# Optimization experiments

Hardware: AMD Instinct MI355X
Metric: run time of the kernel (lower is better)

The kernel has to match this reference:

```python
import jax, jax.numpy as jnp
import numpy as np

HEAD_NUM = 16
QKV_DIM = 32
EMB = 512
SQRT_EMB = 22.627416997969522  # sqrt(512)
LOGIT_CLIP = 10.0
BATCH, POMO, PROBLEM = 32, 256, 1024


def setup_inputs() -> dict:
    key = jax.random.key(0)
    ks = jax.random.split(key, 8)
    s = 0.02
    return {
        "encoded_nodes": jax.random.normal(ks[0], (BATCH, PROBLEM, EMB), jnp.float32),
        "encoded_q1": jax.random.normal(ks[1], (BATCH, POMO, EMB), jnp.float32),
        "encoded_last_node": jax.random.normal(ks[2], (BATCH, POMO, EMB), jnp.float32),
        "ninf_mask": jnp.zeros((BATCH, POMO, PROBLEM), jnp.float32),
        # weights stored [in, out] so y = x @ W (equiv. to torch Linear with W.T)
        "Wq_first": jax.random.normal(ks[3], (EMB, HEAD_NUM * QKV_DIM), jnp.float32) * s,
        "Wq_last": jax.random.normal(ks[4], (EMB, HEAD_NUM * QKV_DIM), jnp.float32) * s,
        "Wk": jax.random.normal(ks[5], (EMB, HEAD_NUM * QKV_DIM), jnp.float32) * s,
        "Wv": jax.random.normal(ks[6], (EMB, HEAD_NUM * QKV_DIM), jnp.float32) * s,
        "W_combine": jax.random.normal(ks[7], (HEAD_NUM * QKV_DIM, EMB), jnp.float32) * s,
        "b_combine": jnp.zeros((EMB,), jnp.float32),
    }


def _heads(x):
    # [b, n, h*d] -> [b, h, n, d]
    b, n, _ = x.shape
    return x.reshape(b, n, HEAD_NUM, QKV_DIM).transpose(0, 2, 1, 3)


def reference(encoded_nodes, encoded_q1, encoded_last_node, ninf_mask,
              Wq_first, Wq_last, Wk, Wv, W_combine, b_combine):
    # set_kv
    k = _heads(encoded_nodes @ Wk)                     # [b,h,problem,d]
    v = _heads(encoded_nodes @ Wv)                     # [b,h,problem,d]
    single_head_key = encoded_nodes.transpose(0, 2, 1) # [b,emb,problem]
    # set_q1
    q_first = _heads(encoded_q1 @ Wq_first)            # [b,h,pomo,d]
    # forward
    q_last = _heads(encoded_last_node @ Wq_last)       # [b,h,pomo,d]
    q = q_first + q_last

    scale = 1.0 / jnp.sqrt(jnp.asarray(QKV_DIM, q.dtype))
    score = jnp.einsum("bhnd,bhmd->bhnm", q, k) * scale  # [b,h,pomo,problem]
    score = score + ninf_mask[:, None, :, :]
    weights = jax.nn.softmax(score, axis=-1)
    out = jnp.einsum("bhnm,bhmd->bhnd", weights, v)      # [b,h,pomo,d]
    out_concat = out.transpose(0, 2, 1, 3).reshape(q.shape[0], q.shape[2], HEAD_NUM * QKV_DIM)
    mh_out = out_concat @ W_combine + b_combine          # [b,pomo,emb]

    score2 = jnp.einsum("bne,bem->bnm", mh_out, single_head_key) / SQRT_EMB
    score2 = LOGIT_CLIP * jnp.tanh(score2) + ninf_mask
    probs = jax.nn.softmax(score2, axis=2)               # [b,pomo,problem]
    return probs
```

## Files before the change

### kernel.cpp

```cpp
#include <hip/hip_runtime.h>
#include <math.h>

typedef unsigned short u16;
typedef __attribute__((ext_vector_type(8))) short bf16x8;
typedef __attribute__((ext_vector_type(4))) float f32x4;
typedef __attribute__((ext_vector_type(4))) int i32x4;
typedef __attribute__((ext_vector_type(4))) short s16x4;
typedef __attribute__((ext_vector_type(4))) unsigned short u16x4;

#define MFMA16(a,b,c) __builtin_amdgcn_mfma_f32_16x16x32_bf16((a),(b),(c),0,0,0)

__device__ __forceinline__ u16 f2bf(float x){
  unsigned int u = __float_as_uint(x);
  u += 0x7fffu + ((u >> 16) & 1u);
  return (u16)(u >> 16);
}
__device__ __forceinline__ float bf2f(u16 x){
  return __uint_as_float(((unsigned)x) << 16);
}
__device__ __forceinline__ void gload16(const void* g, void* l){
  __builtin_amdgcn_global_load_lds((const __attribute__((address_space(1))) void*)g,
                                   (__attribute__((address_space(3))) void*)l, 16, 0, 0);
}

__global__ __launch_bounds__(256) void prep(
    const float* __restrict__ nodes, const float* __restrict__ q1, const float* __restrict__ lastn,
    const float* __restrict__ mask,
    const float* __restrict__ Wqf, const float* __restrict__ Wql, const float* __restrict__ Wk,
    const float* __restrict__ Wv, const float* __restrict__ Wc,
    u16* __restrict__ nodesb, u16* __restrict__ qlb,
    u16* __restrict__ WtKV, u16* __restrict__ WtQ2, u16* __restrict__ WtC,
    u16* __restrict__ maskP)
{
  const int tid = blockIdx.x * 256 + threadIdx.x;
  const int NT = 1048576;
  for (int i = tid; i < 4194304; i += NT) {
    float4 v = ((const float4*)nodes)[i];
    u16x4 o; o[0]=f2bf(v.x); o[1]=f2bf(v.y); o[2]=f2bf(v.z); o[3]=f2bf(v.w);
    *(u16x4*)&nodesb[i*4] = o;
  }
  {
    const int m = tid >> 7, k4 = (tid & 127)*4;
    float4 v = ((const float4*)q1)[tid];
    u16x4 o; o[0]=f2bf(v.x); o[1]=f2bf(v.y); o[2]=f2bf(v.z); o[3]=f2bf(v.w);
    *(u16x4*)&qlb[m*1024 + k4] = o;
    v = ((const float4*)lastn)[tid];
    o[0]=f2bf(v.x); o[1]=f2bf(v.y); o[2]=f2bf(v.z); o[3]=f2bf(v.w);
    *(u16x4*)&qlb[m*1024 + 512 + k4] = o;
  }
  if (tid < 262144) {
    int n = tid >> 9, k = tid & 511;
    WtQ2[n*1024 + k]       = f2bf(Wqf[k*512 + n]);
    WtQ2[n*1024 + 512 + k] = f2bf(Wql[k*512 + n]);
    WtC[tid]  = f2bf(Wc[k*512 + n]);
  }
  if (tid < 524288) {
    int n = tid >> 9, k = tid & 511;
    WtKV[tid] = f2bf(n < 512 ? Wk[k*512 + n] : Wv[k*512 + (n-512)]);
  }
  if (tid < 524288) {
    int brt = tid >> 10, c = tid & 1023;
    const float* mp = mask + (brt*16)*1024 + c;
    u16 vals[16];
    #pragma unroll
    for (int p=0;p<16;p++) vals[p] = f2bf(mp[p*1024]);
    *(i32x4*)&maskP[tid*16]     = *(i32x4*)&vals[0];
    *(i32x4*)&maskP[tid*16 + 8] = *(i32x4*)&vals[8];
  }
}

__global__ __launch_bounds__(512, 2) void kvq(
    const u16* __restrict__ Akv, const u16* __restrict__ Bkv,
    const u16* __restrict__ Aq,  const u16* __restrict__ Bq,
    u16* __restrict__ Kout, u16* __restrict__ Vout, u16* __restrict__ Qout)
{
  __shared__ u16 smem[24576];
  const int t = threadIdx.x, w = t >> 6, l = t & 63, q = l >> 4, ln = l & 15;
  const int wr = w >> 2, wc = w & 3;
  const int wm = wr * 64, wn = wc * 64;

  const bool isq = blockIdx.x < 128;
  int mb, nb, ksteps, kstr;
  const u16 *Ab, *Bb;
  if (isq) {
    const int bid = blockIdx.x;
    mb = bid >> 1; nb = bid & 1;
    ksteps = 32; kstr = 1024; Ab = Aq; Bb = Bq;
  } else {
    const int bid = blockIdx.x - 128;
    mb = (bid >> 5)*8 + (bid & 7);
    nb = (bid >> 3) & 3;
    ksteps = 16; kstr = 512; Ab = Akv; Bb = Bkv;
  }
  const int m0 = mb*128, n0 = nb*256;

  f32x4 acc[4][4];
  #pragma unroll
  for (int i=0;i<4;i++)
    #pragma unroll
    for (int j=0;j<4;j++)
      #pragma unroll
      for (int r=0;r<4;r++) acc[i][j][r] = 0.f;

  const u16* Aaddr = Ab + (m0 + (t & 127))*kstr + (t >> 7)*8;
  const u16* Baddr = Bb + (n0 + (t & 255))*kstr + (t >> 8)*8;

  #define STAGE(kc_, b_) { \
    u16* s = smem + (b_)*12288; \
    gload16(Aaddr + (kc_)*32,      &s[t*8]); \
    gload16(Baddr + (kc_)*32,      &s[4096 + t*8]); \
    gload16(Baddr + 16 + (kc_)*32, &s[4096 + (t+512)*8]); }

  STAGE(0, 0);
  for (int kc = 0; kc < ksteps; kc++) {
    __syncthreads();
    if (kc + 1 < ksteps) STAGE(kc+1, (kc+1)&1);
    const u16* sa = smem + (kc&1)*12288;
    const u16* sb = sa + 4096;
    bf16x8 af[4], bfr[4];
    #pragma unroll
    for (int i=0;i<4;i++) af[i]  = *(bf16x8*)&sa[(q*128 + wm + i*16 + ln)*8];
    #pragma unroll
    for (int j=0;j<4;j++) bfr[j] = *(bf16x8*)&sb[(q*256 + wn + j*16 + ln)*8];
    #pragma unroll
    for (int i=0;i<4;i++)
      #pragma unroll
      for (int j=0;j<4;j++)
        acc[i][j] = MFMA16(af[i], bfr[j], acc[i][j]);
  }
  #undef STAGE

  const float scale = isq ? 0.17677669529663687f : 1.0f;
  const int bb_ = mb >> 3, mloc = (mb & 7)*128;
  const int bbq = mb >> 1, pm0 = (mb & 1)*128;
  for (int h = 0; h < 4; ++h) {
    __syncthreads();
    if (wc == h) {
      #pragma unroll
      for (int i=0;i<4;i++)
        #pragma unroll
        for (int j=0;j<4;j++) {
          s16x4 o;
          #pragma unroll
          for (int r=0;r<4;r++) o[r] = (short)f2bf(acc[i][j][r]*scale);
          *(s16x4*)&smem[(j*16 + ln)*140 + wm + i*16 + q*4] = o;
        }
    }
    __syncthreads();
    #pragma unroll
    for (int hc=0; hc<2; ++hc) {
      if (isq) {
        const int head = nb*8 + h*2 + hc;
        const int m_ = t >> 2, d0 = (t & 3)*8;
        u16 v[8];
        #pragma unroll
        for (int dd=0;dd<8;dd++) v[dd] = smem[(hc*32 + d0 + dd)*140 + m_];
        *(i32x4*)&Qout[((bbq*16 + head)*256 + pm0 + m_)*32 + d0] = *(i32x4*)&v[0];
      } else if (nb < 2) {
        const int head = nb*8 + h*2 + hc;
        const int m_ = t >> 2, d0 = (t & 3)*8;
        u16 v[8];
        #pragma unroll
        for (int dd=0;dd<8;dd++) v[dd] = smem[(hc*32 + d0 + dd)*140 + m_];
        *(i32x4*)&Kout[((bb_*16 + head)*1024 + mloc + m_)*32 + d0] = *(i32x4*)&v[0];
      } else {
        const int vh = (nb-2)*8 + h*2 + hc;
        const int d = t >> 4, mo = (t & 15)*8;
        *(i32x4*)&Vout[((bb_*16 + vh)*32 + d)*1024 + mloc + mo]
            = *(i32x4*)&smem[(hc*32 + d)*140 + mo];
      }
    }
  }
}

__global__ __launch_bounds__(256) void attn(const u16* __restrict__ Qg, const u16* __restrict__ Kg,
                                            const u16* __restrict__ Vtg, const u16* __restrict__ maskP,
                                            u16* __restrict__ Og)
{
  const int bid = blockIdx.x;
  const int bh = (bid & 7)*64 + (bid >> 3);
  const int h = bh & 15, bb = bh >> 4;
  const int t = threadIdx.x, w = t >> 6, l = t & 63, q = l >> 4, ln = l & 15;
  __shared__ u16 Qs[8192];
  __shared__ u16 Ks[4096];
  __shared__ u16 Vs[4096];
  __shared__ u16 Ps[2560];
  u16* Pw = &Ps[w*640];
  const int qbase = (bb*16 + h)*256*32;
  #pragma unroll
  for (int c=0;c<4;c++)
    gload16(&Qg[qbase + t*32 + c*8], &Qs[(c*256 + t)*8]);
  const int kbase = (bb*16 + h)*1024*32;
  const int vbase = (bb*16 + h)*32*1024;
  float rs[4][4];
  f32x4 oacc[4][2];
  #pragma unroll
  for (int rg=0;rg<4;rg++) {
    #pragma unroll
    for (int r=0;r<4;r++) rs[rg][r] = 0.f;
    #pragma unroll
    for (int dt=0;dt<2;dt++)
      #pragma unroll
      for (int r=0;r<4;r++) oacc[rg][dt][r] = 0.f;
  }
  __syncthreads();
  bf16x8 aq[4];
  #pragma unroll
  for (int rg=0;rg<4;rg++) aq[rg] = *(bf16x8*)&Qs[(q*256 + w*64 + rg*16 + ln)*8];
  const u16* mbase = maskP + (bb*16 + w*4)*16384 + q*4;
  u16x4 mqA[8], mqB[8];

  #define RG_BODY(rg, MQC, MQN) { \
    if ((rg) < 3) { \
      _Pragma("unroll") \
      for (int j2=0;j2<8;j2++) \
        MQN[j2] = *(const u16x4*)&mbase[((rg)+1)*16384 + (mc*128 + j2*16 + ln)*16]; \
    } \
    _Pragma("unroll") \
    for (int ch=0; ch<4; ch++) { \
      bf16x8 bk0 = *(bf16x8*)&Ks[(q*128 + (ch*2+0)*16 + ln)*8]; \
      bf16x8 bk1 = *(bf16x8*)&Ks[(q*128 + (ch*2+1)*16 + ln)*8]; \
      f32x4 zz = {0.f,0.f,0.f,0.f}; \
      f32x4 s0 = MFMA16(aq[rg], bk0, zz); \
      f32x4 s1 = MFMA16(aq[rg], bk1, zz); \
      _Pragma("unroll") \
      for (int r=0;r<4;r++) { \
        float e0 = __expf(s0[r] + bf2f(MQC[ch*2+0][r])); \
        float e1 = __expf(s1[r] + bf2f(MQC[ch*2+1][r])); \
        rs[rg][r] += e0 + e1; \
        Pw[(q*4+r)*40 + ln]      = f2bf(e0); \
        Pw[(q*4+r)*40 + 16 + ln] = f2bf(e1); \
      } \
      bf16x8 ap  = *(bf16x8*)&Pw[ln*40 + q*8]; \
      bf16x8 bv0 = *(bf16x8*)&Vs[((ch*4+q)*32 + ln)*8]; \
      bf16x8 bv1 = *(bf16x8*)&Vs[((ch*4+q)*32 + 16 + ln)*8]; \
      oacc[rg][0] = MFMA16(ap, bv0, oacc[rg][0]); \
      oacc[rg][1] = MFMA16(ap, bv1, oacc[rg][1]); \
    } }

  for (int mc = 0; mc < 8; mc++) {
    __syncthreads();
    gload16(&Kg[kbase + (mc*128 + (t & 127))*32 + (t >> 7)*8],       &Ks[t*8]);
    gload16(&Kg[kbase + (mc*128 + (t & 127))*32 + ((t >> 7)+2)*8],   &Ks[(t+256)*8]);
    gload16(&Vtg[vbase + (t & 31)*1024 + mc*128 + (t >> 5)*8],       &Vs[t*8]);
    gload16(&Vtg[vbase + (t & 31)*1024 + mc*128 + ((t >> 5)+8)*8],   &Vs[(t+256)*8]);
    #pragma unroll
    for (int j2=0;j2<8;j2++)
      mqA[j2] = *(const u16x4*)&mbase[(mc*128 + j2*16 + ln)*16];
    __syncthreads();
    RG_BODY(0, mqA, mqB)
    RG_BODY(1, mqB, mqA)
    RG_BODY(2, mqA, mqB)
    RG_BODY(3, mqB, mqA)
  }
  #undef RG_BODY

  #pragma unroll
  for (int rg=0;rg<4;rg++) {
    #pragma unroll
    for (int r=0;r<4;r++) {
      float v = rs[rg][r];
      v += __shfl_xor(v,1); v += __shfl_xor(v,2); v += __shfl_xor(v,4); v += __shfl_xor(v,8);
      rs[rg][r] = __builtin_amdgcn_rcpf(v);
    }
    const int orow = bb*256 + w*64 + rg*16 + q*4;
    #pragma unroll
    for (int dt=0;dt<2;dt++)
      #pragma unroll
      for (int r=0;r<4;r++)
        Og[(orow + r)*512 + h*32 + dt*16 + ln] = f2bf(oacc[rg][dt][r]*rs[rg][r]);
  }
}

__global__ __launch_bounds__(1024) void cmbfin(const u16* __restrict__ oc, const u16* __restrict__ WtC,
                                               const float* __restrict__ bias,
                                               const u16* __restrict__ nodesb, const u16* __restrict__ maskP,
                                               float* __restrict__ out)
{
  const int bid = blockIdx.x;
  const int bb = bid & 31, rg = bid >> 5;
  const int t = threadIdx.x, w = t >> 6, l = t & 63, q = l >> 4, ln = l & 15;
  __shared__ u16 As[16384];
  __shared__ u16 Ms[16384];
  __shared__ float rsL[16][32];
  const int abase = (bb*256 + rg*32)*512;
  #pragma unroll
  for (int c=0;c<2;c++) {
    int chunk = t + 1024*c;
    gload16(&oc[abase + (chunk & 31)*512 + (chunk >> 5)*8], &As[chunk*8]);
  }
  __syncthreads();
  f32x4 acc1[2][2];
  #pragma unroll
  for (int i=0;i<2;i++)
    #pragma unroll
    for (int ct=0;ct<2;ct++)
      #pragma unroll
      for (int r=0;r<4;r++) acc1[i][ct][r] = 0.f;
  for (int kc=0;kc<16;kc++) {
    bf16x8 af[2];
    #pragma unroll
    for (int i=0;i<2;i++) af[i] = *(bf16x8*)&As[((kc*4 + q)*32 + i*16 + ln)*8];
    #pragma unroll
    for (int ct=0;ct<2;ct++) {
      int col = w*32 + ct*16 + ln;
      bf16x8 bfr = *(const bf16x8*)&WtC[col*512 + kc*32 + q*8];
      #pragma unroll
      for (int i=0;i<2;i++) acc1[i][ct] = MFMA16(af[i], bfr, acc1[i][ct]);
    }
  }
  #pragma unroll
  for (int ct=0;ct<2;ct++) {
    int gn = w*32 + ct*16 + ln;
    float bv = bias[gn];
    #pragma unroll
    for (int i=0;i<2;i++)
      #pragma unroll
      for (int r=0;r<4;r++)
        Ms[(gn >> 3)*256 + (i*16 + q*4 + r)*8 + (gn & 7)] = f2bf(acc1[i][ct][r] + bv);
  }
  __syncthreads();
  float rloc[2][4] = {{0.f,0.f,0.f,0.f},{0.f,0.f,0.f,0.f}};
  const int nbase = bb*524288;
  f32x4 acc[2][4];
  #pragma unroll
  for (int i=0;i<2;i++)
    #pragma unroll
    for (int ct=0;ct<4;ct++)
      #pragma unroll
      for (int r=0;r<4;r++) acc[i][ct][r] = 0.f;
  for (int kc=0;kc<16;kc++) {
    bf16x8 af[2];
    #pragma unroll
    for (int i=0;i<2;i++) af[i] = *(bf16x8*)&Ms[((kc*4 + q)*32 + i*16 + ln)*8];
    #pragma unroll
    for (int ct=0;ct<4;ct++) {
      int col = w*64 + ct*16 + ln;
      bf16x8 bfr = *(const bf16x8*)&nodesb[nbase + col*512 + kc*32 + q*8];
      #pragma unroll
      for (int i=0;i<2;i++) acc[i][ct] = MFMA16(af[i], bfr, acc[i][ct]);
    }
  }
  const float c2 = 0.08838834764831843f;
  const int prow_base = bb*256 + rg*32;
  #pragma unroll
  for (int i=0;i<2;i++) {
    #pragma unroll
    for (int ct=0;ct<4;ct++) {
      int col0 = w*64 + ct*16 + ln;
      u16x4 mv = *(const u16x4*)&maskP[((bb*16 + rg*2 + i)*1024 + col0)*16 + q*4];
      #pragma unroll
      for (int r=0;r<4;r++) {
        float x = acc[i][ct][r] * c2;
        x = fminf(fmaxf(x, -30.f), 30.f);
        float e2 = __expf(x);
        float lg = 10.f*(e2 - 1.f)*__builtin_amdgcn_rcpf(e2 + 1.f) + bf2f(mv[r]);
        float e = __expf(lg);
        rloc[i][r] += e;
        acc[i][ct][r] = e;
      }
    }
  }
  #pragma unroll
  for (int i=0;i<2;i++)
    #pragma unroll
    for (int r=0;r<4;r++) {
      float v = rloc[i][r];
      v += __shfl_xor(v,1); v += __shfl_xor(v,2); v += __shfl_xor(v,4); v += __shfl_xor(v,8);
      rloc[i][r] = v;
    }
  if (ln == 0) {
    #pragma unroll
    for (int i=0;i<2;i++)
      #pragma unroll
      for (int r=0;r<4;r++) rsL[w][i*16 + q*4 + r] = rloc[i][r];
  }
  __syncthreads();
  float inv[2][4];
  #pragma unroll
  for (int i=0;i<2;i++)
    #pragma unroll
    for (int r=0;r<4;r++) {
      float tot = 0.f;
      #pragma unroll
      for (int ww=0;ww<16;ww++) tot += rsL[ww][i*16 + q*4 + r];
      inv[i][r] = __builtin_amdgcn_rcpf(tot);
    }
  #pragma unroll
  for (int i=0;i<2;i++)
    #pragma unroll
    for (int ct=0;ct<4;ct++) {
      int col0 = w*64 + ct*16 + ln;
      #pragma unroll
      for (int r=0;r<4;r++)
        out[(prow_base + i*16 + q*4 + r)*1024 + col0] = acc[i][ct][r]*inv[i][r];
    }
}

extern "C" void kernel_launch(void* const* d_in, const int* in_sizes, int n_in,
                              void* d_out, int out_size, void* d_ws, size_t ws_size,
                              hipStream_t stream)
{
  (void)in_sizes; (void)n_in; (void)out_size; (void)ws_size;
  const float* nodes = (const float*)d_in[0];
  const float* q1    = (const float*)d_in[1];
  const float* lastn = (const float*)d_in[2];
  const float* mask  = (const float*)d_in[3];
  const float* Wqf   = (const float*)d_in[4];
  const float* Wql   = (const float*)d_in[5];
  const float* Wk    = (const float*)d_in[6];
  const float* Wv    = (const float*)d_in[7];
  const float* Wc    = (const float*)d_in[8];
  const float* bias  = (const float*)d_in[9];
  float* out = (float*)d_out;

  char* p = (char*)d_ws;
  u16* nodesb = (u16*)p; p += 33554432;
  u16* qlb    = (u16*)p; p += 16777216;
  u16* WtKV   = (u16*)p; p += 1048576;
  u16* WtQ2   = (u16*)p; p += 1048576;
  u16* WtC    = (u16*)p; p += 524288;
  u16* Kt     = (u16*)p; p += 33554432;
  u16* Vt     = (u16*)p; p += 33554432;
  u16* Qh     = (u16*)p; p += 8388608;
  u16* maskP  = (u16*)p; p += 16777216;
  u16* oc  = qlb;

  prep<<<4096, 256, 0, stream>>>(nodes, q1, lastn, mask, Wqf, Wql, Wk, Wv, Wc,
                                 nodesb, qlb, WtKV, WtQ2, WtC, maskP);
  kvq<<<1152, 512, 0, stream>>>(nodesb, WtKV, qlb, WtQ2, Kt, Vt, Qh);
  attn<<<512, 256, 0, stream>>>(Qh, Kt, Vt, maskP, oc);
  cmbfin<<<256, 1024, 0, stream>>>(oc, WtC, bias, nodesb, maskP, out);
}
```

Measured before the change: 374.4 us.

## Pre-pack nodes, queries, W_combine and mask into MFMA fragment-order layouts

```diff
diff --git a/kernel.cpp b/kernel.cpp
--- a/kernel.cpp
+++ b/kernel.cpp
@@ -28,35 +28,50 @@
     const float* __restrict__ mask,
     const float* __restrict__ Wqf, const float* __restrict__ Wql, const float* __restrict__ Wk,
     const float* __restrict__ Wv, const float* __restrict__ Wc,
-    u16* __restrict__ nodesb, u16* __restrict__ qlb,
-    u16* __restrict__ WtKV, u16* __restrict__ WtQ2, u16* __restrict__ WtC,
-    u16* __restrict__ maskP)
+    u16* __restrict__ qlbP,
+    u16* __restrict__ WtKV, u16* __restrict__ WtQ2, u16* __restrict__ WtCP,
+    u16* __restrict__ nodesP, u16* __restrict__ maskP)
 {
   const int tid = blockIdx.x * 256 + threadIdx.x;
-  const int NT = 1048576;
-  for (int i = tid; i < 4194304; i += NT) {
-    float4 v = ((const float4*)nodes)[i];
-    u16x4 o; o[0]=f2bf(v.x); o[1]=f2bf(v.y); o[2]=f2bf(v.z); o[3]=f2bf(v.w);
-    *(u16x4*)&nodesb[i*4] = o;
-  }
+
+  #pragma unroll
+  for (int it = 0; it < 2; ++it) {
+    int id = tid + it*1048576;
+    int ln = id & 15, q = (id >> 4) & 3, kc = (id >> 6) & 15, cb = (id >> 10) & 63, b = id >> 16;
+    const float* s = nodes + ((b*1024 + cb*16 + ln)*512 + kc*32 + q*8);
+    float4 v0 = *(const float4*)s, v1 = *(const float4*)(s+4);
+    u16 o[8];
+    o[0]=f2bf(v0.x); o[1]=f2bf(v0.y); o[2]=f2bf(v0.z); o[3]=f2bf(v0.w);
+    o[4]=f2bf(v1.x); o[5]=f2bf(v1.y); o[6]=f2bf(v1.z); o[7]=f2bf(v1.w);
+    *(i32x4*)&nodesP[id*8] = *(i32x4*)&o[0];
+  }
+
   {
-    const int m = tid >> 7, k4 = (tid & 127)*4;
-    float4 v = ((const float4*)q1)[tid];
-    u16x4 o; o[0]=f2bf(v.x); o[1]=f2bf(v.y); o[2]=f2bf(v.z); o[3]=f2bf(v.w);
-    *(u16x4*)&qlb[m*1024 + k4] = o;
-    v = ((const float4*)lastn)[tid];
-    o[0]=f2bf(v.x); o[1]=f2bf(v.y); o[2]=f2bf(v.z); o[3]=f2bf(v.w);
-    *(u16x4*)&qlb[m*1024 + 512 + k4] = o;
-  }
+    int ln = tid & 15, q = (tid >> 4) & 3, kc = (tid >> 6) & 31, mblk = tid >> 11;
+    int m = mblk*16 + ln, k = kc*32 + q*8;
+    const float* s = (k < 512) ? (q1 + m*512 + k) : (lastn + m*512 + (k - 512));
+    float4 v0 = *(const float4*)s, v1 = *(const float4*)(s+4);
+    u16 o[8];
+    o[0]=f2bf(v0.x); o[1]=f2bf(v0.y); o[2]=f2bf(v0.z); o[3]=f2bf(v0.w);
+    o[4]=f2bf(v1.x); o[5]=f2bf(v1.y); o[6]=f2bf(v1.z); o[7]=f2bf(v1.w);
+    *(i32x4*)&qlbP[tid*8] = *(i32x4*)&o[0];
+  }
+
   if (tid < 262144) {
     int n = tid >> 9, k = tid & 511;
     WtQ2[n*1024 + k]       = f2bf(Wqf[k*512 + n]);
     WtQ2[n*1024 + 512 + k] = f2bf(Wql[k*512 + n]);
-    WtC[tid]  = f2bf(Wc[k*512 + n]);
   }
   if (tid < 524288) {
     int n = tid >> 9, k = tid & 511;
     WtKV[tid] = f2bf(n < 512 ? Wk[k*512 + n] : Wv[k*512 + (n-512)]);
+  }
+  if (tid < 32768) {
+    int ln = tid & 15, q = (tid >> 4) & 3, kc = (tid >> 6) & 15, cb = tid >> 10;
+    u16 o[8];
+    #pragma unroll
+    for (int e=0;e<8;e++) o[e] = f2bf(Wc[(kc*32 + q*8 + e)*512 + cb*16 + ln]);
+    *(i32x4*)&WtCP[tid*8] = *(i32x4*)&o[0];
   }
   if (tid < 524288) {
     int brt = tid >> 10, c = tid & 1023;
@@ -64,8 +79,12 @@
     u16 vals[16];
     #pragma unroll
     for (int p=0;p<16;p++) vals[p] = f2bf(mp[p*1024]);
-    *(i32x4*)&maskP[tid*16]     = *(i32x4*)&vals[0];
-    *(i32x4*)&maskP[tid*16 + 8] = *(i32x4*)&vals[8];
+    u16* dst = maskP + (brt*64 + (c >> 4))*256 + (c & 15)*4;
+    #pragma unroll
+    for (int q4=0;q4<4;q4++) {
+      u16x4 v; v[0]=vals[q4*4]; v[1]=vals[q4*4+1]; v[2]=vals[q4*4+2]; v[3]=vals[q4*4+3];
+      *(u16x4*)&dst[q4*64] = v;
+    }
   }
 }
 
@@ -80,17 +99,17 @@
   const int wm = wr * 64, wn = wc * 64;
 
   const bool isq = blockIdx.x < 128;
-  int mb, nb, ksteps, kstr;
+  int mb, nb, ksteps, kstr, KC;
   const u16 *Ab, *Bb;
   if (isq) {
     const int bid = blockIdx.x;
     mb = bid >> 1; nb = bid & 1;
-    ksteps = 32; kstr = 1024; Ab = Aq; Bb = Bq;
+    ksteps = 32; kstr = 1024; KC = 32; Ab = Aq; Bb = Bq;
   } else {
     const int bid = blockIdx.x - 128;
     mb = (bid >> 5)*8 + (bid & 7);
     nb = (bid >> 3) & 3;
-    ksteps = 16; kstr = 512; Ab = Akv; Bb = Bkv;
+    ksteps = 16; kstr = 512; KC = 16; Ab = Akv; Bb = Bkv;
   }
   const int m0 = mb*128, n0 = nb*256;
 
@@ -102,12 +121,12 @@
       #pragma unroll
       for (int r=0;r<4;r++) acc[i][j][r] = 0.f;
 
-  const u16* Aaddr = Ab + (m0 + (t & 127))*kstr + (t >> 7)*8;
+  const u16* ApL  = Ab + (((m0 >> 4) + (t >> 6))*KC*64 + (t & 63))*8;
   const u16* Baddr = Bb + (n0 + (t & 255))*kstr + (t >> 8)*8;
 
   #define STAGE(kc_, b_) { \
     u16* s = smem + (b_)*12288; \
-    gload16(Aaddr + (kc_)*32,      &s[t*8]); \
+    gload16(ApL + (kc_)*512,       &s[t*8]); \
     gload16(Baddr + (kc_)*32,      &s[4096 + t*8]); \
     gload16(Baddr + 16 + (kc_)*32, &s[4096 + (t+512)*8]); }
 
@@ -117,9 +136,10 @@
     if (kc + 1 < ksteps) STAGE(kc+1, (kc+1)&1);
     const u16* sa = smem + (kc&1)*12288;
     const u16* sb = sa + 4096;
+    const int acb = wm >> 4;
     bf16x8 af[4], bfr[4];
     #pragma unroll
-    for (int i=0;i<4;i++) af[i]  = *(bf16x8*)&sa[(q*128 + wm + i*16 + ln)*8];
+    for (int i=0;i<4;i++) af[i]  = *(bf16x8*)&sa[((acb + i)*4 + q)*128 + ln*8];
     #pragma unroll
     for (int j=0;j<4;j++) bfr[j] = *(bf16x8*)&sb[(q*256 + wn + j*16 + ln)*8];
     #pragma unroll
@@ -207,14 +227,14 @@
   bf16x8 aq[4];
   #pragma unroll
   for (int rg=0;rg<4;rg++) aq[rg] = *(bf16x8*)&Qs[(q*256 + w*64 + rg*16 + ln)*8];
-  const u16* mbase = maskP + (bb*16 + w*4)*16384 + q*4;
+  const u16* mbase = maskP + (bb*16 + w*4)*16384 + q*64 + ln*4;
   u16x4 mqA[8], mqB[8];
 
   #define RG_BODY(rg, MQC, MQN) { \
     if ((rg) < 3) { \
       _Pragma("unroll") \
       for (int j2=0;j2<8;j2++) \
-        MQN[j2] = *(const u16x4*)&mbase[((rg)+1)*16384 + (mc*128 + j2*16 + ln)*16]; \
+        MQN[j2] = *(const u16x4*)&mbase[((rg)+1)*16384 + (mc*8 + j2)*256]; \
     } \
     _Pragma("unroll") \
     for (int ch=0; ch<4; ch++) { \
@@ -246,7 +266,7 @@
     gload16(&Vtg[vbase + (t & 31)*1024 + mc*128 + ((t >> 5)+8)*8],   &Vs[(t+256)*8]);
     #pragma unroll
     for (int j2=0;j2<8;j2++)
-      mqA[j2] = *(const u16x4*)&mbase[(mc*128 + j2*16 + ln)*16];
+      mqA[j2] = *(const u16x4*)&mbase[(mc*8 + j2)*256];
     __syncthreads();
     RG_BODY(0, mqA, mqB)
     RG_BODY(1, mqB, mqA)
@@ -272,9 +292,9 @@
   }
 }
 
-__global__ __launch_bounds__(1024) void cmbfin(const u16* __restrict__ oc, const u16* __restrict__ WtC,
+__global__ __launch_bounds__(1024) void cmbfin(const u16* __restrict__ oc, const u16* __restrict__ WtCP,
                                                const float* __restrict__ bias,
-                                               const u16* __restrict__ nodesb, const u16* __restrict__ maskP,
+                                               const u16* __restrict__ nodesP, const u16* __restrict__ maskP,
                                                float* __restrict__ out)
 {
   const int bid = blockIdx.x;
@@ -303,8 +323,7 @@
     for (int i=0;i<2;i++) af[i] = *(bf16x8*)&As[((kc*4 + q)*32 + i*16 + ln)*8];
     #pragma unroll
     for (int ct=0;ct<2;ct++) {
-      int col = w*32 + ct*16 + ln;
-      bf16x8 bfr = *(const bf16x8*)&WtC[col*512 + kc*32 + q*8];
+      bf16x8 bfr = *(const bf16x8*)&WtCP[(((w*2 + ct)*16 + kc)*4 + q)*128 + ln*8];
       #pragma unroll
       for (int i=0;i<2;i++) acc1[i][ct] = MFMA16(af[i], bfr, acc1[i][ct]);
     }
@@ -335,8 +354,7 @@
     for (int i=0;i<2;i++) af[i] = *(bf16x8*)&Ms[((kc*4 + q)*32 + i*16 + ln)*8];
     #pragma unroll
     for (int ct=0;ct<4;ct++) {
-      int col = w*64 + ct*16 + ln;
-      bf16x8 bfr = *(const bf16x8*)&nodesb[nbase + col*512 + kc*32 + q*8];
+      bf16x8 bfr = *(const bf16x8*)&nodesP[nbase + (((w*4 + ct)*16 + kc)*4 + q)*128 + ln*8];
       #pragma unroll
       for (int i=0;i<2;i++) acc[i][ct] = MFMA16(af[i], bfr, acc[i][ct]);
     }
@@ -347,8 +365,7 @@
   for (int i=0;i<2;i++) {
     #pragma unroll
     for (int ct=0;ct<4;ct++) {
-      int col0 = w*64 + ct*16 + ln;
-      u16x4 mv = *(const u16x4*)&maskP[((bb*16 + rg*2 + i)*1024 + col0)*16 + q*4];
+      u16x4 mv = *(const u16x4*)&maskP[((bb*16 + rg*2 + i)*64 + w*4 + ct)*256 + q*64 + ln*4];
       #pragma unroll
       for (int r=0;r<4;r++) {
         float x = acc[i][ct][r] * c2;
@@ -415,20 +432,20 @@
   float* out = (float*)d_out;
 
   char* p = (char*)d_ws;
-  u16* nodesb = (u16*)p; p += 33554432;
-  u16* qlb    = (u16*)p; p += 16777216;
+  u16* qlbP   = (u16*)p; p += 16777216;
   u16* WtKV   = (u16*)p; p += 1048576;
   u16* WtQ2   = (u16*)p; p += 1048576;
-  u16* WtC    = (u16*)p; p += 524288;
+  u16* WtCP   = (u16*)p; p += 524288;
+  u16* nodesP = (u16*)p; p += 33554432;
+  u16* maskP  = (u16*)p; p += 16777216;
   u16* Kt     = (u16*)p; p += 33554432;
   u16* Vt     = (u16*)p; p += 33554432;
   u16* Qh     = (u16*)p; p += 8388608;
-  u16* maskP  = (u16*)p; p += 16777216;
-  u16* oc  = qlb;
+  u16* oc  = qlbP;
 
   prep<<<4096, 256, 0, stream>>>(nodes, q1, lastn, mask, Wqf, Wql, Wk, Wv, Wc,
-                                 nodesb, qlb, WtKV, WtQ2, WtC, maskP);
-  kvq<<<1152, 512, 0, stream>>>(nodesb, WtKV, qlb, WtQ2, Kt, Vt, Qh);
+                                 qlbP, WtKV, WtQ2, WtCP, nodesP, maskP);
+  kvq<<<1152, 512, 0, stream>>>(nodesP, WtKV, qlbP, WtQ2, Kt, Vt, Qh);
   attn<<<512, 256, 0, stream>>>(Qh, Kt, Vt, maskP, oc);
-  cmbfin<<<256, 1024, 0, stream>>>(oc, WtC, bias, nodesb, maskP, out);
-}
+  cmbfin<<<256, 1024, 0, stream>>>(oc, WtCP, bias, nodesP, maskP, out);
+}
```

Measured after the change: 342.1 us. 1.09x faster.
